# Kernel tuning notes

Hardware: AMD Instinct MI355X
Metric: run time of the kernel (lower is better)

The kernel has to match this reference:

```python
import jax, jax.numpy as jnp
import numpy as np
import math

N_HEADS = 16
FACTOR = 5

def setup_inputs() -> dict:
    key = jax.random.key(0)
    ks = jax.random.split(key, 9)
    B, T, D = 4, 2048, 1024
    w = lambda k: jax.random.normal(k, (D, D), dtype=jnp.float32) * 0.02
    return {
        "x": jax.random.normal(ks[0], (B, T, D), dtype=jnp.float32),
        "Wq": w(ks[1]), "bq": jnp.zeros((D,), jnp.float32),
        "Wk": w(ks[2]), "bk": jnp.zeros((D,), jnp.float32),
        "Wv": w(ks[3]), "bv": jnp.zeros((D,), jnp.float32),
        "Wo": w(ks[4]), "bo": jnp.zeros((D,), jnp.float32),
    }

def reference(x, Wq, bq, Wk, bk, Wv, bv, Wo, bo):
    B, T, D = x.shape
    H = N_HEADS
    hd = D // H
    scale = hd ** (-0.5)

    def proj(W, b):
        # [B,T,D] -> [B,H,T,hd]
        return (x @ W + b).reshape(B, T, H, hd).transpose(0, 2, 1, 3)

    q = proj(Wq, bq)
    k = proj(Wk, bk)
    v = proj(Wv, bv)

    # top-u query selection by L1 norm per (b,h)
    u = min(int(FACTOR * math.log(T)), T)
    q_norm = jnp.sum(jnp.abs(q), axis=-1)          # [B,H,T]
    _, idx = jax.lax.top_k(q_norm, u)              # [B,H,u]

    # gather selected queries; compute only the u selected score rows
    q_sel = jnp.take_along_axis(q, idx[..., None], axis=2)  # [B,H,u,hd]
    sel_scores = jnp.einsum('bhud,bhtd->bhut', q_sel, k) * scale  # [B,H,u,T]

    # causal mask for selected rows: key pos j attends iff j <= query pos
    causal = jnp.arange(T)[None, None, None, :] <= idx[..., None]  # [B,H,u,T]
    sel_scores = jnp.where(causal, sel_scores, -jnp.inf)

    attn = jax.nn.softmax(sel_scores, axis=-1)     # dropout omitted (eval)
    sel_out = jnp.einsum('bhut,bhtd->bhud', attn, v)  # [B,H,u,hd]

    # scatter selected rows back into zeros (non-selected rows stay 0)
    bi = jnp.arange(B)[:, None, None]
    hi = jnp.arange(H)[None, :, None]
    attn_out = jnp.zeros((B, H, T, hd), x.dtype).at[bi, hi, idx].set(sel_out)

    out = attn_out.transpose(0, 2, 1, 3).reshape(B, T, D)
    return out @ Wo + bo
```

## Files before the change

kernel.cpp:

```cpp
#include <hip/hip_runtime.h>
#include <hip/hip_bf16.h>
#include <math.h>

#define B_  4
#define T_  2048
#define D_  1024
#define H_  16
#define HD_ 64
#define U_  38
#define M_  (B_*T_)
#define NCB_ 8
#define NC_ 144

typedef __attribute__((ext_vector_type(8))) short bf16x8;
typedef __attribute__((ext_vector_type(4))) float f32x4;

__device__ __forceinline__ short f2b(float f) {
    __hip_bfloat16 b = __float2bfloat16(f);
    return *(short*)&b;
}
__device__ __forceinline__ float b2f(short s) {
    __hip_bfloat16 b = *(__hip_bfloat16*)&s;
    return __bfloat162float(b);
}
__device__ __forceinline__ unsigned pack2(float lo, float hi) {
    unsigned a = (unsigned short)f2b(lo);
    unsigned b = ((unsigned)(unsigned short)f2b(hi)) << 16;
    return a | b;
}

__device__ __forceinline__ void gload16(const void* g, void* l) {
    __builtin_amdgcn_global_load_lds(
        (const __attribute__((address_space(1))) unsigned int*)g,
        (__attribute__((address_space(3))) unsigned int*)l,
        16, 0, 0);
}

__global__ __launch_bounds__(256) void conv_fused(
    const float* __restrict__ x,
    const float* __restrict__ Wq, const float* __restrict__ Wk,
    const float* __restrict__ Wv, const float* __restrict__ Wo,
    short* __restrict__ xh, short* __restrict__ xl,
    short* __restrict__ wq2, short* __restrict__ wkvt, short* __restrict__ wot)
{
    __shared__ float tile[32][33];
    const int bid = blockIdx.x;
    if (bid < 8192) {
        const size_t i = ((size_t)bid * 256 + threadIdx.x) * 4;
        float4 v = *(const float4*)(x + i);
        short4 h, l;
        h.x = f2b(v.x); l.x = f2b(v.x - b2f(h.x));
        h.y = f2b(v.y); l.y = f2b(v.y - b2f(h.y));
        h.z = f2b(v.z); l.z = f2b(v.z - b2f(h.z));
        h.w = f2b(v.w); l.w = f2b(v.w - b2f(h.w));
        *(short4*)(xh + i) = h;
        *(short4*)(xl + i) = l;
        return;
    }
    const int q = bid - 8192;
    const int which = q >> 10;
    const int by = (q & 1023) >> 5, bx = q & 31;
    const float* W = which == 0 ? Wq : (which == 1 ? Wk : (which == 2 ? Wv : Wo));
    const int k0 = by * 32, n0 = bx * 32;
    const int tx = threadIdx.x & 31, ty = threadIdx.x >> 5;
    #pragma unroll
    for (int r = ty; r < 32; r += 8)
        tile[r][tx] = W[(size_t)(k0 + r) * D_ + n0 + tx];
    __syncthreads();
    #pragma unroll
    for (int r = ty; r < 32; r += 8) {
        float v = tile[tx][r];
        size_t o = (size_t)(n0 + r) * D_ + k0 + tx;
        if (which == 0) {
            short h = f2b(v);
            wq2[o] = h;
            wq2[o + 1048576] = f2b(v - b2f(h));
        } else if (which == 3) {
            wot[o] = f2b(v);
        } else {
            wkvt[(size_t)(which - 1) * D_ * D_ + o] = f2b(v);
        }
    }
}

__global__ __launch_bounds__(256) void gemm_fused(
    const short* __restrict__ xh, const short* __restrict__ wq2,
    const short* __restrict__ wkvt,
    const float* __restrict__ bq, const float* __restrict__ bk,
    const float* __restrict__ bv,
    float* __restrict__ qnorm, short* __restrict__ kb, short* __restrict__ vt)
{
    __shared__ short As[128 * 64];
    __shared__ short Bs[128 * 64];
    const int bid = blockIdx.x;
    const bool isQ = bid < 512;
    const int tid = threadIdx.x, wid = tid >> 6, lane = tid & 63;
    const int l15 = lane & 15, gr = lane >> 4;
    const int lb = isQ ? bid : bid - 512;
    const int m0 = (lb & 63) * 128;
    const int n0 = (lb >> 6) * 128;
    const bool isK = !isQ && (n0 < D_);
    const int wr = (wid >> 1) * 64, wc = (wid & 1) * 64;

    f32x4 acc[4][4];
    #pragma unroll
    for (int i = 0; i < 4; ++i)
        #pragma unroll
        for (int j = 0; j < 4; ++j)
            acc[i][j] = (f32x4){0.f, 0.f, 0.f, 0.f};

    const short* Asrc = xh;
    const short* Bsrc = isQ ? wq2 : wkvt;

    for (int kt = 0; kt < 16; ++kt) {
        const int ka = kt * 64;
        #pragma unroll
        for (int i = 0; i < 4; ++i) {
            const int e = tid + i * 256;
            const int row = e >> 3;
            const int soff = ((e & 7) ^ (row & 7)) * 8;
            gload16(Asrc + (size_t)(m0 + row) * D_ + ka + soff,
                    (char*)As + i * 4096 + wid * 1024);
            gload16(Bsrc + (size_t)(n0 + row) * D_ + ka + soff,
                    (char*)Bs + i * 4096 + wid * 1024);
        }
        __syncthreads();
        #pragma unroll
        for (int ks = 0; ks < 2; ++ks) {
            bf16x8 a[4], b[4];
            #pragma unroll
            for (int i = 0; i < 4; ++i)
                a[i] = *(bf16x8*)((char*)As + (wr + i * 16 + l15) * 128
                                   + (((ks << 2) | gr) ^ (l15 & 7)) * 16);
            #pragma unroll
            for (int j = 0; j < 4; ++j)
                b[j] = *(bf16x8*)((char*)Bs + (wc + j * 16 + l15) * 128
                                   + (((ks << 2) | gr) ^ (l15 & 7)) * 16);
            if (isK) {
                #pragma unroll
                for (int i = 0; i < 4; ++i)
                    #pragma unroll
                    for (int j = 0; j < 4; ++j)
                        acc[i][j] = __builtin_amdgcn_mfma_f32_16x16x32_bf16(b[j], a[i], acc[i][j], 0, 0, 0);
            } else {
                #pragma unroll
                for (int i = 0; i < 4; ++i)
                    #pragma unroll
                    for (int j = 0; j < 4; ++j)
                        acc[i][j] = __builtin_amdgcn_mfma_f32_16x16x32_bf16(a[i], b[j], acc[i][j], 0, 0, 0);
            }
        }
        __syncthreads();
    }

    if (isQ) {
        const int h = (n0 + wc) >> 6;
        #pragma unroll
        for (int i = 0; i < 4; ++i)
            #pragma unroll
            for (int r = 0; r < 4; ++r) {
                int row = m0 + wr + i * 16 + gr * 4 + r;
                float s = 0.f;
                #pragma unroll
                for (int j = 0; j < 4; ++j) {
                    int col = n0 + wc + j * 16 + l15;
                    s += fabsf(acc[i][j][r] + bq[col]);
                }
                s += __shfl_xor(s, 1);
                s += __shfl_xor(s, 2);
                s += __shfl_xor(s, 4);
                s += __shfl_xor(s, 8);
                if (l15 == 0) {
                    int b = row >> 11, t = row & (T_ - 1);
                    qnorm[((size_t)b * H_ + h) * T_ + t] = s;
                }
            }
    } else if (isK) {
        #pragma unroll
        for (int i = 0; i < 4; ++i)
            #pragma unroll
            for (int j = 0; j < 4; ++j) {
                const int m = m0 + wr + i * 16 + l15;
                const int bb = m >> 11, t = m & (T_ - 1);
                const int n = n0 + wc + j * 16 + gr * 4;
                const int hh = n >> 6, dd = n & 63;
                float4 bias = *(const float4*)(bk + n);
                short4 pk;
                pk.x = f2b(acc[i][j][0] + bias.x);
                pk.y = f2b(acc[i][j][1] + bias.y);
                pk.z = f2b(acc[i][j][2] + bias.z);
                pk.w = f2b(acc[i][j][3] + bias.w);
                *(short4*)(kb + (((size_t)bb * H_ + hh) * T_ + t) * HD_ + dd) = pk;
            }
    } else {
        #pragma unroll
        for (int i = 0; i < 4; ++i)
            #pragma unroll
            for (int j = 0; j < 4; ++j) {
                const int col = n0 + wc + j * 16 + l15;
                const int rowb = m0 + wr + i * 16 + gr * 4;
                const int bb = rowb >> 11, t0 = rowb & (T_ - 1);
                const int cc2 = col - D_;
                const int hh = cc2 >> 6, dd = cc2 & 63;
                const float bias = bv[cc2];
                short4 pk;
                pk.x = f2b(acc[i][j][0] + bias);
                pk.y = f2b(acc[i][j][1] + bias);
                pk.z = f2b(acc[i][j][2] + bias);
                pk.w = f2b(acc[i][j][3] + bias);
                *(short4*)(vt + (((size_t)bb * H_ + hh) * HD_ + dd) * T_ + t0) = pk;
            }
    }
}

__global__ __launch_bounds__(64) void cand_kernel(
    const float* __restrict__ qnorm, int* __restrict__ cand)
{
    const int g = blockIdx.x;
    const int lane = threadIdx.x;
    unsigned v[32];
    const float* src = qnorm + (size_t)g * T_ + lane * 32;
    #pragma unroll
    for (int i = 0; i < 32; i += 4) {
        float4 t = *(const float4*)(src + i);
        v[i] = __float_as_uint(t.x); v[i + 1] = __float_as_uint(t.y);
        v[i + 2] = __float_as_uint(t.z); v[i + 3] = __float_as_uint(t.w);
    }
    unsigned lo = 0, hi = 0x7F800000u;
    while (lo < hi) {
        unsigned mid = lo + ((hi - lo) >> 1);
        int c = 0;
        #pragma unroll
        for (int i = 0; i < 32; ++i) c += (v[i] >= mid) ? 1 : 0;
        #pragma unroll
        for (int off = 1; off < 64; off <<= 1) c += __shfl_xor(c, off);
        if (c <= NC_) hi = mid; else lo = mid + 1;
    }
    const unsigned tau = lo;
    int myc = 0;
    #pragma unroll
    for (int i = 0; i < 32; ++i) myc += (v[i] >= tau) ? 1 : 0;
    int inc = myc;
    for (int off = 1; off < 64; off <<= 1) {
        int n = __shfl_up(inc, off);
        if (lane >= off) inc += n;
    }
    const int total = __shfl(inc, 63);
    int pos = inc - myc;
    #pragma unroll
    for (int i = 0; i < 32; ++i)
        if (v[i] >= tau) cand[g * NC_ + pos++] = lane * 32 + i;
    for (int p = total + lane; p < NC_; p += 64)
        cand[g * NC_ + p] = -1;
}

__global__ __launch_bounds__(64) void recheck_kernel(
    const short* __restrict__ xh, const short* __restrict__ xl,
    const short* __restrict__ wq2, const float* __restrict__ bq,
    const int* __restrict__ cand,
    float* __restrict__ cnorm, short* __restrict__ candq)
{
    const int blk = blockIdx.x;
    const int g = blk / 9, rt = blk % 9;
    const int b = g >> 4, h = g & 15;
    const int lane = threadIdx.x, l15 = lane & 15, gr = lane >> 4;

    const int aslot = rt * 16 + l15;
    int at = cand[g * NC_ + aslot];
    const size_t arow = ((size_t)b * T_ + (at < 0 ? 0 : at)) * D_;

    f32x4 acc[4];
    #pragma unroll
    for (int j = 0; j < 4; ++j) acc[j] = (f32x4){0.f, 0.f, 0.f, 0.f};

    const short* wqh = wq2;
    const short* wql = wq2 + 1048576;
    for (int kt = 0; kt < 32; ++kt) {
        const int k0 = kt * 32 + gr * 8;
        bf16x8 ah = *(const bf16x8*)(xh + arow + k0);
        bf16x8 al = *(const bf16x8*)(xl + arow + k0);
        #pragma unroll
        for (int j = 0; j < 4; ++j) {
            const size_t wrow = (size_t)(h * HD_ + j * 16 + l15) * D_ + k0;
            bf16x8 bh = *(const bf16x8*)(wqh + wrow);
            bf16x8 bl = *(const bf16x8*)(wql + wrow);
            acc[j] = __builtin_amdgcn_mfma_f32_16x16x32_bf16(ah, bh, acc[j], 0, 0, 0);
            acc[j] = __builtin_amdgcn_mfma_f32_16x16x32_bf16(ah, bl, acc[j], 0, 0, 0);
            acc[j] = __builtin_amdgcn_mfma_f32_16x16x32_bf16(al, bh, acc[j], 0, 0, 0);
        }
    }

    #pragma unroll
    for (int r = 0; r < 4; ++r) {
        const int slot = rt * 16 + gr * 4 + r;
        float s = 0.f;
        #pragma unroll
        for (int j = 0; j < 4; ++j) {
            const int col = j * 16 + l15;
            float val = acc[j][r] + bq[h * HD_ + col];
            candq[((size_t)g * NC_ + slot) * HD_ + col] = f2b(val);
            s += fabsf(val);
        }
        s += __shfl_xor(s, 1);
        s += __shfl_xor(s, 2);
        s += __shfl_xor(s, 4);
        s += __shfl_xor(s, 8);
        if (l15 == 0) {
            int ct = cand[g * NC_ + slot];
            cnorm[g * NC_ + slot] = (ct < 0) ? -3e38f : s;
        }
    }
}

__global__ __launch_bounds__(64) void topk38_kernel(
    const float* __restrict__ cnorm, const int* __restrict__ cand,
    int* __restrict__ idxb, int* __restrict__ slotb)
{
    const int g = blockIdx.x;
    const int lane = threadIdx.x;
    float v[3]; int tt[3];
    #pragma unroll
    for (int i = 0; i < 3; ++i) {
        int s = lane + 64 * i;
        if (s < NC_) {
            v[i] = cnorm[g * NC_ + s];
            int c = cand[g * NC_ + s];
            tt[i] = (c < 0) ? (1 << 30) : c;
            if (c < 0) v[i] = -3e38f;
        } else { v[i] = -3e38f; tt[i] = 1 << 30; }
    }
    for (int it = 0; it < U_; ++it) {
        float bv = -3e38f; int bt = 1 << 30, bi = 0;
        #pragma unroll
        for (int i = 0; i < 3; ++i) {
            bool better = (v[i] > bv) || (v[i] == bv && tt[i] < bt);
            if (better) { bv = v[i]; bt = tt[i]; bi = i; }
        }
        int bs = lane + 64 * bi;
        for (int off = 32; off; off >>= 1) {
            float ov = __shfl_xor(bv, off);
            int ot = __shfl_xor(bt, off);
            int os = __shfl_xor(bs, off);
            if (ov > bv || (ov == bv && ot < bt)) { bv = ov; bt = ot; bs = os; }
        }
        if (lane == 0) { idxb[g * U_ + it] = bt; slotb[g * 40 + it] = bs; }
        if ((bs & 63) == lane) {
            int wi = bs >> 6;
            if (wi == 0) v[0] = -3e38f;
            else if (wi == 1) v[1] = -3e38f;
            else v[2] = -3e38f;
        }
    }
}

__global__ __launch_bounds__(256) void attn_part(
    const short* __restrict__ candq, const int* __restrict__ slotb,
    const short* __restrict__ kb, const short* __restrict__ vt,
    const int* __restrict__ idxb,
    float* __restrict__ pm, float* __restrict__ pl, float* __restrict__ po)
{
    __shared__ short qs[48 * 72];
    __shared__ __align__(16) char shbuf[40448];
    __shared__ int sidx[48];
    short* pls  = (short*)shbuf;
    float* redo = (float*)shbuf;
    float* redm = (float*)(shbuf + 38912);
    float* redl = (float*)(shbuf + 39680);

    const int bid = blockIdx.x;
    const int g = bid & 63;
    const int c = bid >> 6;
    const int tid = threadIdx.x, wid = tid >> 6, lane = tid & 63;
    const int l15 = lane & 15, gr = lane >> 4;
    const int j0w = (c * 4 + wid) * 64;

    if (tid < 48) sidx[tid] = (tid < U_) ? idxb[g * U_ + tid] : 0;
    __syncthreads();
    for (int e = tid; e < 48 * 16; e += 256) {
        int u = e >> 4, d4 = e & 15;
        short4 v = make_short4(0, 0, 0, 0);
        if (u < U_) {
            int slot = slotb[g * 40 + u];
            v = *(const short4*)(candq + ((size_t)g * NC_ + slot) * HD_ + d4 * 4);
        }
        *(short4*)&qs[u * 72 + d4 * 4] = v;
    }
    __syncthreads();

    int su[3];
    #pragma unroll
    for (int uf = 0; uf < 3; ++uf) su[uf] = sidx[uf * 16 + l15];

    f32x4 accs[3][4];
    #pragma unroll
    for (int uf = 0; uf < 3; ++uf)
        #pragma unroll
        for (int jf = 0; jf < 4; ++jf)
            accs[uf][jf] = (f32x4){0.f, 0.f, 0.f, 0.f};

    bf16x8 ka[4][2], qb[3][2];
    #pragma unroll
    for (int jf = 0; jf < 4; ++jf)
        #pragma unroll
        for (int ks = 0; ks < 2; ++ks)
            ka[jf][ks] = *(const bf16x8*)(kb + ((size_t)g * T_ + j0w + jf * 16 + l15) * HD_ + ks * 32 + gr * 8);
    #pragma unroll
    for (int uf = 0; uf < 3; ++uf)
        #pragma unroll
        for (int ks = 0; ks < 2; ++ks)
            qb[uf][ks] = *(bf16x8*)&qs[(uf * 16 + l15) * 72 + ks * 32 + gr * 8];

    #pragma unroll
    for (int uf = 0; uf < 3; ++uf)
        #pragma unroll
        for (int jf = 0; jf < 4; ++jf) {
            accs[uf][jf] = __builtin_amdgcn_mfma_f32_16x16x32_bf16(ka[jf][0], qb[uf][0], accs[uf][jf], 0, 0, 0);
            accs[uf][jf] = __builtin_amdgcn_mfma_f32_16x16x32_bf16(ka[jf][1], qb[uf][1], accs[uf][jf], 0, 0, 0);
        }

    #pragma unroll
    for (int uf = 0; uf < 3; ++uf) {
        float mm = -3e38f;
        #pragma unroll
        for (int jf = 0; jf < 4; ++jf)
            #pragma unroll
            for (int r = 0; r < 4; ++r) {
                int j = j0w + jf * 16 + gr * 4 + r;
                float s = accs[uf][jf][r] * 0.125f;
                s = (j <= su[uf]) ? s : -1e30f;
                accs[uf][jf][r] = s;
                mm = fmaxf(mm, s);
            }
        mm = fmaxf(mm, __shfl_xor(mm, 16));
        mm = fmaxf(mm, __shfl_xor(mm, 32));
        float ll = 0.f;
        #pragma unroll
        for (int jf = 0; jf < 4; ++jf)
            #pragma unroll
            for (int r = 0; r < 4; ++r) {
                float e = __expf(accs[uf][jf][r] - mm);
                accs[uf][jf][r] = e;
                ll += e;
            }
        ll += __shfl_xor(ll, 16);
        ll += __shfl_xor(ll, 32);
        if (gr == 0) {
            int u = uf * 16 + l15;
            redm[wid * 48 + u] = mm;
            redl[wid * 48 + u] = ll;
        }
    }

    short* pw = pls + wid * 48 * 72;
    #pragma unroll
    for (int uf = 0; uf < 3; ++uf)
        #pragma unroll
        for (int jf = 0; jf < 4; ++jf) {
            uint2 wv;
            wv.x = pack2(accs[uf][jf][0], accs[uf][jf][1]);
            wv.y = pack2(accs[uf][jf][2], accs[uf][jf][3]);
            *(uint2*)&pw[(uf * 16 + l15) * 72 + jf * 16 + gr * 4] = wv;
        }

    bf16x8 va[4][2], pb[3][2];
    #pragma unroll
    for (int df = 0; df < 4; ++df)
        #pragma unroll
        for (int ks = 0; ks < 2; ++ks)
            va[df][ks] = *(const bf16x8*)(vt + ((size_t)g * HD_ + df * 16 + l15) * T_ + j0w + ks * 32 + gr * 8);
    #pragma unroll
    for (int uf = 0; uf < 3; ++uf)
        #pragma unroll
        for (int ks = 0; ks < 2; ++ks)
            pb[uf][ks] = *(bf16x8*)&pw[(uf * 16 + l15) * 72 + ks * 32 + gr * 8];

    f32x4 acco[4][3];
    #pragma unroll
    for (int df = 0; df < 4; ++df)
        #pragma unroll
        for (int uf = 0; uf < 3; ++uf)
            acco[df][uf] = (f32x4){0.f, 0.f, 0.f, 0.f};
    #pragma unroll
    for (int df = 0; df < 4; ++df)
        #pragma unroll
        for (int uf = 0; uf < 3; ++uf) {
            acco[df][uf] = __builtin_amdgcn_mfma_f32_16x16x32_bf16(va[df][0], pb[uf][0], acco[df][uf], 0, 0, 0);
            acco[df][uf] = __builtin_amdgcn_mfma_f32_16x16x32_bf16(va[df][1], pb[uf][1], acco[df][uf], 0, 0, 0);
        }

    __syncthreads();

    #pragma unroll
    for (int df = 0; df < 4; ++df)
        #pragma unroll
        for (int uf = 0; uf < 3; ++uf) {
            int u = uf * 16 + l15;
            if (u < U_) {
                float4 o;
                o.x = acco[df][uf][0]; o.y = acco[df][uf][1];
                o.z = acco[df][uf][2]; o.w = acco[df][uf][3];
                *(float4*)&redo[((size_t)(wid * 38 + u)) * 64 + df * 16 + gr * 4] = o;
            }
        }
    __syncthreads();

    for (int e = tid; e < U_ * 64; e += 256) {
        int u = e >> 6, d = e & 63;
        float m0 = redm[u], m1 = redm[48 + u], m2 = redm[96 + u], m3 = redm[144 + u];
        float m = fmaxf(fmaxf(m0, m1), fmaxf(m2, m3));
        float e0 = __expf(m0 - m), e1 = __expf(m1 - m), e2 = __expf(m2 - m), e3 = __expf(m3 - m);
        float l = redl[u] * e0 + redl[48 + u] * e1 + redl[96 + u] * e2 + redl[144 + u] * e3;
        float o = redo[(size_t)u * 64 + d] * e0
                + redo[(size_t)(38 + u) * 64 + d] * e1
                + redo[(size_t)(76 + u) * 64 + d] * e2
                + redo[(size_t)(114 + u) * 64 + d] * e3;
        po[((size_t)(g * NCB_ + c) * U_ + u) * HD_ + d] = o;
        if (d == 0) {
            pm[(size_t)(g * NCB_ + c) * U_ + u] = m;
            pl[(size_t)(g * NCB_ + c) * U_ + u] = l;
        }
    }
}

__global__ __launch_bounds__(256) void attn_combine(
    const float* __restrict__ pm, const float* __restrict__ pl,
    const float* __restrict__ po, float* __restrict__ selo)
{
    const int g = blockIdx.x;
    const int u = blockIdx.y * 4 + (threadIdx.x >> 6);
    const int d = threadIdx.x & 63;
    if (u >= U_) return;

    const float* pmg = pm + (size_t)g * NCB_ * U_ + u;
    const float* plg = pl + (size_t)g * NCB_ * U_ + u;

    float mc[NCB_];
    #pragma unroll
    for (int c = 0; c < NCB_; ++c) mc[c] = pmg[(size_t)c * U_];
    float m = -3e38f;
    #pragma unroll
    for (int c = 0; c < NCB_; ++c) m = fmaxf(m, mc[c]);

    float w[NCB_];
    #pragma unroll
    for (int c = 0; c < NCB_; ++c) w[c] = __expf(mc[c] - m);

    float l = 0.f;
    #pragma unroll
    for (int c = 0; c < NCB_; ++c) l += plg[(size_t)c * U_] * w[c];

    float o = 0.f;
    #pragma unroll
    for (int c = 0; c < NCB_; ++c)
        o += po[(((size_t)g * NCB_ + c) * U_ + u) * HD_ + d] * w[c];

    selo[((size_t)g * U_ + u) * HD_ + d] = o / l;
}

__global__ __launch_bounds__(256) void fill_kernel(
    const float* __restrict__ bo, float* __restrict__ out)
{
    const size_t i = (size_t)blockIdx.x * 256 + threadIdx.x;
    float4 bv = *(const float4*)(bo + ((i & 255) << 2));
    *(float4*)(out + i * 4) = bv;
}

__global__ __launch_bounds__(256) void oproj_kernel(
    const float* __restrict__ selo, const int* __restrict__ idxb,
    const short* __restrict__ wot, float* __restrict__ out)
{
    __shared__ short sel[48 * 72];
    __shared__ int st[48];
    const int g = blockIdx.x;
    const int b = g >> 4, h = g & 15;
    const int tid = threadIdx.x, w = tid >> 6, lane = tid & 63;
    const int l15 = lane & 15, gr = lane >> 4;

    for (int e = tid; e < 48 * 16; e += 256) {
        int u = e >> 4, d4 = e & 15;
        short4 v4 = make_short4(0, 0, 0, 0);
        if (u < U_) {
            float4 f = *(const float4*)(selo + ((size_t)g * U_ + u) * HD_ + d4 * 4);
            v4.x = f2b(f.x); v4.y = f2b(f.y); v4.z = f2b(f.z); v4.w = f2b(f.w);
        }
        *(short4*)&sel[u * 72 + d4 * 4] = v4;
    }
    if (tid < 48) st[tid] = (tid < U_) ? idxb[g * U_ + tid] : 0;
    __syncthreads();

    bf16x8 a[3][2];
    #pragma unroll
    for (int uf = 0; uf < 3; ++uf)
        #pragma unroll
        for (int ks = 0; ks < 2; ++ks)
            a[uf][ks] = *(bf16x8*)&sel[(uf * 16 + l15) * 72 + ks * 32 + gr * 8];

    for (int nf = 0; nf < 16; ++nf) {
        const int n0 = w * 256 + nf * 16;
        bf16x8 bf[2];
        #pragma unroll
        for (int ks = 0; ks < 2; ++ks)
            bf[ks] = *(const bf16x8*)(wot + (size_t)(n0 + l15) * D_ + h * HD_ + ks * 32 + gr * 8);
        f32x4 acc[3];
        #pragma unroll
        for (int uf = 0; uf < 3; ++uf) {
            acc[uf] = (f32x4){0.f, 0.f, 0.f, 0.f};
            acc[uf] = __builtin_amdgcn_mfma_f32_16x16x32_bf16(a[uf][0], bf[0], acc[uf], 0, 0, 0);
            acc[uf] = __builtin_amdgcn_mfma_f32_16x16x32_bf16(a[uf][1], bf[1], acc[uf], 0, 0, 0);
        }
        #pragma unroll
        for (int uf = 0; uf < 3; ++uf)
            #pragma unroll
            for (int r = 0; r < 4; ++r) {
                int u = uf * 16 + gr * 4 + r;
                if (u < U_)
                    atomicAdd(out + ((size_t)b * T_ + st[u]) * D_ + n0 + l15, acc[uf][r]);
            }
    }
}

extern "C" void kernel_launch(void* const* d_in, const int* in_sizes, int n_in,
                              void* d_out, int out_size, void* d_ws, size_t ws_size,
                              hipStream_t stream)
{
    const float* x  = (const float*)d_in[0];
    const float* Wq = (const float*)d_in[1];
    const float* bq = (const float*)d_in[2];
    const float* Wk = (const float*)d_in[3];
    const float* bk = (const float*)d_in[4];
    const float* Wv = (const float*)d_in[5];
    const float* bv = (const float*)d_in[6];
    const float* Wo = (const float*)d_in[7];
    const float* bo = (const float*)d_in[8];
    float* out = (float*)d_out;

    char* ws = (char*)d_ws;
    short* xh    = (short*)(ws);
    short* xl    = (short*)(ws + 16777216);
    short* wq2   = (short*)(ws + 33554432);
    short* wkvt  = (short*)(ws + 37748736);
    short* kb    = (short*)(ws + 41943040);
    short* vt    = (short*)(ws + 58720256);
    float* qnorm = (float*)(ws + 75497472);
    int*   idxb  = (int*)  (ws + 76021760);
    float* selo  = (float*)(ws + 76038144);
    int*   cand  = (int*)  (ws + 76660736);
    float* cnorm = (float*)(ws + 76697600);
    int*   slotb = (int*)  (ws + 76734464);
    short* candq = (short*)(ws + 76750848);
    short* wot   = (short*)(ws + 77930496);
    float* po    = (float*)(ws);
    float* pm    = (float*)(ws + 19922944);
    float* pl    = (float*)(ws + 20234240);

    conv_fused<<<8192 + 4096, 256, 0, stream>>>(x, Wq, Wk, Wv, Wo,
                                                xh, xl, wq2, wkvt, wot);
    gemm_fused<<<1536, 256, 0, stream>>>(xh, wq2, wkvt, bq, bk, bv, qnorm, kb, vt);
    cand_kernel<<<B_ * H_, 64, 0, stream>>>(qnorm, cand);
    recheck_kernel<<<B_ * H_ * 9, 64, 0, stream>>>(xh, xl, wq2, bq, cand, cnorm, candq);
    topk38_kernel<<<B_ * H_, 64, 0, stream>>>(cnorm, cand, idxb, slotb);
    attn_part<<<64 * NCB_, 256, 0, stream>>>(candq, slotb, kb, vt, idxb, pm, pl, po);
    attn_combine<<<dim3(B_ * H_, (U_ + 3) / 4), 256, 0, stream>>>(pm, pl, po, selo);
    fill_kernel<<<(M_ * D_ / 4) / 256, 256, 0, stream>>>(bo, out);
    oproj_kernel<<<B_ * H_, 256, 0, stream>>>(selo, idxb, wot, out);
}
```

Before: 199.1 us.

## Shrink candidate pool, fuse fill and combine, skip fully masked attention tiles

Several changes land together. The bias fill of the output moves into the conversion kernel, and the split-softmax combine is folded into the output projection, which removes two kernel launches and the selo round trip. The candidate count for top-k rechecking drops from 144 to 96, cutting recheck blocks and the top-k work, and top-k now writes its results in token order through a ballot. attn_part skips the QK and PV MFMAs for query fragments whose highest selected position lies before the key chunk. A smaller candidate pool risks missing true top-u queries if the bf16 norm ranking used to pick candidates is off.

```diff
diff --git a/kernel.cpp b/kernel.cpp
--- a/kernel.cpp
+++ b/kernel.cpp
@@ -10,7 +10,7 @@
 #define U_  38
 #define M_  (B_*T_)
 #define NCB_ 8
-#define NC_ 144
+#define NC_ 96
 
 typedef __attribute__((ext_vector_type(8))) short bf16x8;
 typedef __attribute__((ext_vector_type(4))) float f32x4;
@@ -40,8 +40,10 @@
     const float* __restrict__ x,
     const float* __restrict__ Wq, const float* __restrict__ Wk,
     const float* __restrict__ Wv, const float* __restrict__ Wo,
+    const float* __restrict__ bo,
     short* __restrict__ xh, short* __restrict__ xl,
-    short* __restrict__ wq2, short* __restrict__ wkvt, short* __restrict__ wot)
+    short* __restrict__ wq2, short* __restrict__ wkvt, short* __restrict__ wot,
+    float* __restrict__ out)
 {
     __shared__ float tile[32][33];
     const int bid = blockIdx.x;
@@ -55,6 +57,12 @@
         h.w = f2b(v.w); l.w = f2b(v.w - b2f(h.w));
         *(short4*)(xh + i) = h;
         *(short4*)(xl + i) = l;
+        return;
+    }
+    if (bid >= 12288) {
+        const size_t i = (size_t)(bid - 12288) * 256 + threadIdx.x;
+        float4 bv = *(const float4*)(bo + ((i & 255) << 2));
+        *(float4*)(out + i * 4) = bv;
         return;
     }
     const int q = bid - 8192;
@@ -261,7 +269,7 @@
     float* __restrict__ cnorm, short* __restrict__ candq)
 {
     const int blk = blockIdx.x;
-    const int g = blk / 9, rt = blk % 9;
+    const int g = blk / 6, rt = blk % 6;
     const int b = g >> 4, h = g & 15;
     const int lane = threadIdx.x, l15 = lane & 15, gr = lane >> 4;
 
@@ -318,9 +326,10 @@
 {
     const int g = blockIdx.x;
     const int lane = threadIdx.x;
-    float v[3]; int tt[3];
-    #pragma unroll
-    for (int i = 0; i < 3; ++i) {
+    float v[2]; int tt[2];
+    bool fl0 = false, fl1 = false;
+    #pragma unroll
+    for (int i = 0; i < 2; ++i) {
         int s = lane + 64 * i;
         if (s < NC_) {
             v[i] = cnorm[g * NC_ + s];
@@ -330,12 +339,9 @@
         } else { v[i] = -3e38f; tt[i] = 1 << 30; }
     }
     for (int it = 0; it < U_; ++it) {
-        float bv = -3e38f; int bt = 1 << 30, bi = 0;
-        #pragma unroll
-        for (int i = 0; i < 3; ++i) {
-            bool better = (v[i] > bv) || (v[i] == bv && tt[i] < bt);
-            if (better) { bv = v[i]; bt = tt[i]; bi = i; }
-        }
+        float bv; int bt, bi;
+        if (v[0] > v[1] || (v[0] == v[1] && tt[0] < tt[1])) { bv = v[0]; bt = tt[0]; bi = 0; }
+        else { bv = v[1]; bt = tt[1]; bi = 1; }
         int bs = lane + 64 * bi;
         for (int off = 32; off; off >>= 1) {
             float ov = __shfl_xor(bv, off);
@@ -343,13 +349,23 @@
             int os = __shfl_xor(bs, off);
             if (ov > bv || (ov == bv && ot < bt)) { bv = ov; bt = ot; bs = os; }
         }
-        if (lane == 0) { idxb[g * U_ + it] = bt; slotb[g * 40 + it] = bs; }
         if ((bs & 63) == lane) {
-            int wi = bs >> 6;
-            if (wi == 0) v[0] = -3e38f;
-            else if (wi == 1) v[1] = -3e38f;
-            else v[2] = -3e38f;
-        }
+            if ((bs >> 6) == 0) { v[0] = -3e38f; fl0 = true; }
+            else                { v[1] = -3e38f; fl1 = true; }
+        }
+    }
+    unsigned long long b0 = __ballot(fl0), b1 = __ballot(fl1);
+    int n0 = __popcll(b0);
+    unsigned long long lowmask = ((unsigned long long)1 << lane) - 1;
+    if (fl0) {
+        int p = __popcll(b0 & lowmask);
+        idxb[g * U_ + p] = tt[0];
+        slotb[g * 40 + p] = lane;
+    }
+    if (fl1) {
+        int p = n0 + __popcll(b1 & lowmask);
+        idxb[g * U_ + p] = tt[1];
+        slotb[g * 40 + p] = lane + 64;
     }
 }
 
@@ -387,6 +403,13 @@
     }
     __syncthreads();
 
+    bool skp[3];
+    #pragma unroll
+    for (int uf = 0; uf < 3; ++uf) {
+        int mi = uf * 16 + 15; if (mi >= U_) mi = U_ - 1;
+        skp[uf] = (sidx[mi] < j0w);
+    }
+
     int su[3];
     #pragma unroll
     for (int uf = 0; uf < 3; ++uf) su[uf] = sidx[uf * 16 + l15];
@@ -398,81 +421,81 @@
         for (int jf = 0; jf < 4; ++jf)
             accs[uf][jf] = (f32x4){0.f, 0.f, 0.f, 0.f};
 
-    bf16x8 ka[4][2], qb[3][2];
+    bf16x8 ka[4][2];
     #pragma unroll
     for (int jf = 0; jf < 4; ++jf)
         #pragma unroll
         for (int ks = 0; ks < 2; ++ks)
             ka[jf][ks] = *(const bf16x8*)(kb + ((size_t)g * T_ + j0w + jf * 16 + l15) * HD_ + ks * 32 + gr * 8);
-    #pragma unroll
-    for (int uf = 0; uf < 3; ++uf)
-        #pragma unroll
-        for (int ks = 0; ks < 2; ++ks)
-            qb[uf][ks] = *(bf16x8*)&qs[(uf * 16 + l15) * 72 + ks * 32 + gr * 8];
-
-    #pragma unroll
-    for (int uf = 0; uf < 3; ++uf)
-        #pragma unroll
-        for (int jf = 0; jf < 4; ++jf) {
-            accs[uf][jf] = __builtin_amdgcn_mfma_f32_16x16x32_bf16(ka[jf][0], qb[uf][0], accs[uf][jf], 0, 0, 0);
-            accs[uf][jf] = __builtin_amdgcn_mfma_f32_16x16x32_bf16(ka[jf][1], qb[uf][1], accs[uf][jf], 0, 0, 0);
-        }
 
     #pragma unroll
     for (int uf = 0; uf < 3; ++uf) {
-        float mm = -3e38f;
-        #pragma unroll
-        for (int jf = 0; jf < 4; ++jf)
-            #pragma unroll
-            for (int r = 0; r < 4; ++r) {
-                int j = j0w + jf * 16 + gr * 4 + r;
-                float s = accs[uf][jf][r] * 0.125f;
-                s = (j <= su[uf]) ? s : -1e30f;
-                accs[uf][jf][r] = s;
-                mm = fmaxf(mm, s);
-            }
-        mm = fmaxf(mm, __shfl_xor(mm, 16));
-        mm = fmaxf(mm, __shfl_xor(mm, 32));
-        float ll = 0.f;
-        #pragma unroll
-        for (int jf = 0; jf < 4; ++jf)
-            #pragma unroll
-            for (int r = 0; r < 4; ++r) {
-                float e = __expf(accs[uf][jf][r] - mm);
-                accs[uf][jf][r] = e;
-                ll += e;
-            }
-        ll += __shfl_xor(ll, 16);
-        ll += __shfl_xor(ll, 32);
-        if (gr == 0) {
-            int u = uf * 16 + l15;
-            redm[wid * 48 + u] = mm;
-            redl[wid * 48 + u] = ll;
+        if (!skp[uf]) {
+            bf16x8 q0 = *(bf16x8*)&qs[(uf * 16 + l15) * 72 + gr * 8];
+            bf16x8 q1 = *(bf16x8*)&qs[(uf * 16 + l15) * 72 + 32 + gr * 8];
+            #pragma unroll
+            for (int jf = 0; jf < 4; ++jf) {
+                accs[uf][jf] = __builtin_amdgcn_mfma_f32_16x16x32_bf16(ka[jf][0], q0, accs[uf][jf], 0, 0, 0);
+                accs[uf][jf] = __builtin_amdgcn_mfma_f32_16x16x32_bf16(ka[jf][1], q1, accs[uf][jf], 0, 0, 0);
+            }
         }
     }
 
     short* pw = pls + wid * 48 * 72;
     #pragma unroll
-    for (int uf = 0; uf < 3; ++uf)
-        #pragma unroll
-        for (int jf = 0; jf < 4; ++jf) {
-            uint2 wv;
-            wv.x = pack2(accs[uf][jf][0], accs[uf][jf][1]);
-            wv.y = pack2(accs[uf][jf][2], accs[uf][jf][3]);
-            *(uint2*)&pw[(uf * 16 + l15) * 72 + jf * 16 + gr * 4] = wv;
-        }
-
-    bf16x8 va[4][2], pb[3][2];
+    for (int uf = 0; uf < 3; ++uf) {
+        if (skp[uf]) {
+            if (gr == 0) {
+                int u = uf * 16 + l15;
+                redm[wid * 48 + u] = -1e30f;
+                redl[wid * 48 + u] = 0.f;
+            }
+        } else {
+            float mm = -3e38f;
+            #pragma unroll
+            for (int jf = 0; jf < 4; ++jf)
+                #pragma unroll
+                for (int r = 0; r < 4; ++r) {
+                    int j = j0w + jf * 16 + gr * 4 + r;
+                    float s = accs[uf][jf][r] * 0.125f;
+                    s = (j <= su[uf]) ? s : -1e30f;
+                    accs[uf][jf][r] = s;
+                    mm = fmaxf(mm, s);
+                }
+            mm = fmaxf(mm, __shfl_xor(mm, 16));
+            mm = fmaxf(mm, __shfl_xor(mm, 32));
+            float ll = 0.f;
+            #pragma unroll
+            for (int jf = 0; jf < 4; ++jf)
+                #pragma unroll
+                for (int r = 0; r < 4; ++r) {
+                    float e = __expf(accs[uf][jf][r] - mm);
+                    accs[uf][jf][r] = e;
+                    ll += e;
+                }
+            ll += __shfl_xor(ll, 16);
+            ll += __shfl_xor(ll, 32);
+            if (gr == 0) {
+                int u = uf * 16 + l15;
+                redm[wid * 48 + u] = mm;
+                redl[wid * 48 + u] = ll;
+            }
+            #pragma unroll
+            for (int jf = 0; jf < 4; ++jf) {
+                uint2 wv;
+                wv.x = pack2(accs[uf][jf][0], accs[uf][jf][1]);
+                wv.y = pack2(accs[uf][jf][2], accs[uf][jf][3]);
+                *(uint2*)&pw[(uf * 16 + l15) * 72 + jf * 16 + gr * 4] = wv;
+            }
+        }
+    }
+
+    bf16x8 va[4][2];
     #pragma unroll
     for (int df = 0; df < 4; ++df)
         #pragma unroll
         for (int ks = 0; ks < 2; ++ks)
             va[df][ks] = *(const bf16x8*)(vt + ((size_t)g * HD_ + df * 16 + l15) * T_ + j0w + ks * 32 + gr * 8);
-    #pragma unroll
-    for (int uf = 0; uf < 3; ++uf)
-        #pragma unroll
-        for (int ks = 0; ks < 2; ++ks)
-            pb[uf][ks] = *(bf16x8*)&pw[(uf * 16 + l15) * 72 + ks * 32 + gr * 8];
 
     f32x4 acco[4][3];
     #pragma unroll
@@ -481,12 +504,17 @@
         for (int uf = 0; uf < 3; ++uf)
             acco[df][uf] = (f32x4){0.f, 0.f, 0.f, 0.f};
     #pragma unroll
-    for (int df = 0; df < 4; ++df)
-        #pragma unroll
-        for (int uf = 0; uf < 3; ++uf) {
-            acco[df][uf] = __builtin_amdgcn_mfma_f32_16x16x32_bf16(va[df][0], pb[uf][0], acco[df][uf], 0, 0, 0);
-            acco[df][uf] = __builtin_amdgcn_mfma_f32_16x16x32_bf16(va[df][1], pb[uf][1], acco[df][uf], 0, 0, 0);
-        }
+    for (int uf = 0; uf < 3; ++uf) {
+        if (!skp[uf]) {
+            bf16x8 p0 = *(bf16x8*)&pw[(uf * 16 + l15) * 72 + gr * 8];
+            bf16x8 p1 = *(bf16x8*)&pw[(uf * 16 + l15) * 72 + 32 + gr * 8];
+            #pragma unroll
+            for (int df = 0; df < 4; ++df) {
+                acco[df][uf] = __builtin_amdgcn_mfma_f32_16x16x32_bf16(va[df][0], p0, acco[df][uf], 0, 0, 0);
+                acco[df][uf] = __builtin_amdgcn_mfma_f32_16x16x32_bf16(va[df][1], p1, acco[df][uf], 0, 0, 0);
+            }
+        }
+    }
 
     __syncthreads();
 
@@ -522,70 +550,51 @@
     }
 }
 
-__global__ __launch_bounds__(256) void attn_combine(
+__global__ __launch_bounds__(256) void oproj_kernel(
     const float* __restrict__ pm, const float* __restrict__ pl,
-    const float* __restrict__ po, float* __restrict__ selo)
-{
-    const int g = blockIdx.x;
-    const int u = blockIdx.y * 4 + (threadIdx.x >> 6);
-    const int d = threadIdx.x & 63;
-    if (u >= U_) return;
-
-    const float* pmg = pm + (size_t)g * NCB_ * U_ + u;
-    const float* plg = pl + (size_t)g * NCB_ * U_ + u;
-
-    float mc[NCB_];
-    #pragma unroll
-    for (int c = 0; c < NCB_; ++c) mc[c] = pmg[(size_t)c * U_];
-    float m = -3e38f;
-    #pragma unroll
-    for (int c = 0; c < NCB_; ++c) m = fmaxf(m, mc[c]);
-
-    float w[NCB_];
-    #pragma unroll
-    for (int c = 0; c < NCB_; ++c) w[c] = __expf(mc[c] - m);
-
-    float l = 0.f;
-    #pragma unroll
-    for (int c = 0; c < NCB_; ++c) l += plg[(size_t)c * U_] * w[c];
-
-    float o = 0.f;
-    #pragma unroll
-    for (int c = 0; c < NCB_; ++c)
-        o += po[(((size_t)g * NCB_ + c) * U_ + u) * HD_ + d] * w[c];
-
-    selo[((size_t)g * U_ + u) * HD_ + d] = o / l;
-}
-
-__global__ __launch_bounds__(256) void fill_kernel(
-    const float* __restrict__ bo, float* __restrict__ out)
-{
-    const size_t i = (size_t)blockIdx.x * 256 + threadIdx.x;
-    float4 bv = *(const float4*)(bo + ((i & 255) << 2));
-    *(float4*)(out + i * 4) = bv;
-}
-
-__global__ __launch_bounds__(256) void oproj_kernel(
-    const float* __restrict__ selo, const int* __restrict__ idxb,
+    const float* __restrict__ po, const int* __restrict__ idxb,
     const short* __restrict__ wot, float* __restrict__ out)
 {
     __shared__ short sel[48 * 72];
     __shared__ int st[48];
+    __shared__ float swl[U_][NCB_];
     const int g = blockIdx.x;
     const int b = g >> 4, h = g & 15;
     const int tid = threadIdx.x, w = tid >> 6, lane = tid & 63;
     const int l15 = lane & 15, gr = lane >> 4;
 
+    if (tid < 48) st[tid] = (tid < U_) ? idxb[g * U_ + tid] : 0;
+    if (tid < U_) {
+        float mc[NCB_], lc[NCB_];
+        #pragma unroll
+        for (int c = 0; c < NCB_; ++c) {
+            mc[c] = pm[(size_t)(g * NCB_ + c) * U_ + tid];
+            lc[c] = pl[(size_t)(g * NCB_ + c) * U_ + tid];
+        }
+        float m = -3e38f;
+        #pragma unroll
+        for (int c = 0; c < NCB_; ++c) m = fmaxf(m, mc[c]);
+        float wv[NCB_], l = 0.f;
+        #pragma unroll
+        for (int c = 0; c < NCB_; ++c) { wv[c] = __expf(mc[c] - m); l += lc[c] * wv[c]; }
+        float inv = 1.f / l;
+        #pragma unroll
+        for (int c = 0; c < NCB_; ++c) swl[tid][c] = wv[c] * inv;
+    }
     for (int e = tid; e < 48 * 16; e += 256) {
         int u = e >> 4, d4 = e & 15;
-        short4 v4 = make_short4(0, 0, 0, 0);
-        if (u < U_) {
-            float4 f = *(const float4*)(selo + ((size_t)g * U_ + u) * HD_ + d4 * 4);
-            v4.x = f2b(f.x); v4.y = f2b(f.y); v4.z = f2b(f.z); v4.w = f2b(f.w);
-        }
-        *(short4*)&sel[u * 72 + d4 * 4] = v4;
-    }
-    if (tid < 48) st[tid] = (tid < U_) ? idxb[g * U_ + tid] : 0;
+        if (u >= U_) *(short4*)&sel[u * 72 + d4 * 4] = make_short4(0, 0, 0, 0);
+    }
+    __syncthreads();
+
+    for (int e = tid; e < U_ * 64; e += 256) {
+        int u = e >> 6, d = e & 63;
+        float o = 0.f;
+        #pragma unroll
+        for (int c = 0; c < NCB_; ++c)
+            o += po[((size_t)(g * NCB_ + c) * U_ + u) * HD_ + d] * swl[u][c];
+        sel[u * 72 + d] = f2b(o);
+    }
     __syncthreads();
 
     bf16x8 a[3][2];
@@ -643,7 +652,6 @@
     short* vt    = (short*)(ws + 58720256);
     float* qnorm = (float*)(ws + 75497472);
     int*   idxb  = (int*)  (ws + 76021760);
-    float* selo  = (float*)(ws + 76038144);
     int*   cand  = (int*)  (ws + 76660736);
     float* cnorm = (float*)(ws + 76697600);
     int*   slotb = (int*)  (ws + 76734464);
@@ -653,14 +661,12 @@
     float* pm    = (float*)(ws + 19922944);
     float* pl    = (float*)(ws + 20234240);
 
-    conv_fused<<<8192 + 4096, 256, 0, stream>>>(x, Wq, Wk, Wv, Wo,
-                                                xh, xl, wq2, wkvt, wot);
+    conv_fused<<<8192 + 4096 + 8192, 256, 0, stream>>>(x, Wq, Wk, Wv, Wo, bo,
+                                                       xh, xl, wq2, wkvt, wot, out);
     gemm_fused<<<1536, 256, 0, stream>>>(xh, wq2, wkvt, bq, bk, bv, qnorm, kb, vt);
     cand_kernel<<<B_ * H_, 64, 0, stream>>>(qnorm, cand);
-    recheck_kernel<<<B_ * H_ * 9, 64, 0, stream>>>(xh, xl, wq2, bq, cand, cnorm, candq);
+    recheck_kernel<<<B_ * H_ * 6, 64, 0, stream>>>(xh, xl, wq2, bq, cand, cnorm, candq);
     topk38_kernel<<<B_ * H_, 64, 0, stream>>>(cnorm, cand, idxb, slotb);
     attn_part<<<64 * NCB_, 256, 0, stream>>>(candq, slotb, kb, vt, idxb, pm, pl, po);
-    attn_combine<<<dim3(B_ * H_, (U_ + 3) / 4), 256, 0, stream>>>(pm, pl, po, selo);
-    fill_kernel<<<(M_ * D_ / 4) / 256, 256, 0, stream>>>(bo, out);
-    oproj_kernel<<<B_ * H_, 256, 0, stream>>>(selo, idxb, wot, out);
-}
+    oproj_kernel<<<B_ * H_, 256, 0, stream>>>(pm, pl, po, idxb, wot, out);
+}
```

After: 185.3 us. 6.9% less time.
